# Kernel tuning notes

Hardware: AMD Instinct MI355X
Metric: run time of the kernel (lower is better)

Reference implementation:

```python
import jax, jax.numpy as jnp
import numpy as np

B, CH, T = 8, 512, 1024
HEADS = 8
KC = CH // HEADS  # 64
BLOCK = 256       # block_length


def setup_inputs() -> dict:
    key = jax.random.key(0)
    ks = jax.random.split(key, 10)
    s = 0.05
    x = jax.random.normal(ks[0], (B, CH, T), jnp.float32)
    c = jax.random.normal(ks[1], (B, CH, T), jnp.float32)
    attn_mask = jnp.ones((1, 1, T, T), jnp.int32)
    # 1x1 Conv1d weights are just [out, in] matrices over the channel dim.
    Wq = jax.random.normal(ks[2], (CH, CH), jnp.float32) * s
    bq = jax.random.normal(ks[3], (CH,), jnp.float32) * s
    Wk = jax.random.normal(ks[4], (CH, CH), jnp.float32) * s
    bk = jax.random.normal(ks[5], (CH,), jnp.float32) * s
    Wv = jax.random.normal(ks[6], (CH, CH), jnp.float32) * s
    bv = jax.random.normal(ks[7], (CH,), jnp.float32) * s
    Wo = jax.random.normal(ks[8], (CH, CH), jnp.float32) * s
    bo = jax.random.normal(ks[9], (CH,), jnp.float32) * s
    return {"x": x, "c": c, "attn_mask": attn_mask,
            "Wq": Wq, "bq": bq, "Wk": Wk, "bk": bk,
            "Wv": Wv, "bv": bv, "Wo": Wo, "bo": bo}


def _proj(W, b, z):
    # 1x1 Conv1d: [B,C,T] -> [B,O,T]
    return jnp.einsum('oc,bct->bot', W, z) + b[None, :, None]


def reference(x, c, attn_mask, Wq, bq, Wk, bk, Wv, bv, Wo, bo):
    q = _proj(Wq, bq, x)
    k = _proj(Wk, bk, c)
    v = _proj(Wv, bv, c)

    def split_heads(z):  # [B,C,T] -> [B,H,T,KC]
        return z.reshape(B, HEADS, KC, T).transpose(0, 1, 3, 2)

    qh, kh, vh = split_heads(q), split_heads(k), split_heads(v)

    scale = jnp.asarray(1.0 / np.sqrt(KC), qh.dtype)
    scores = jnp.einsum('bhtd,bhsd->bhts', qh * scale, kh)  # [B,H,T,T]

    r = jnp.arange(T)
    diff = jnp.abs(r[None, :] - r[:, None])  # |i - j|, [T,T]
    # proximal bias: -log(1 + |i-j|)
    scores = scores + (-jnp.log1p(diff.astype(scores.dtype)))[None, None]
    # attention mask: masked_fill(mask == 0, -1e4)
    scores = jnp.where(attn_mask == 0, jnp.asarray(-1e4, scores.dtype), scores)
    # block-length band mask: keep |i-j| <= BLOCK (triu(-BLOCK).tril(BLOCK))
    band = (diff <= BLOCK)[None, None]
    scores = jnp.where(band, scores, jnp.asarray(-1e4, scores.dtype))

    p_attn = jax.nn.softmax(scores, axis=-1)
    out = jnp.einsum('bhts,bhsd->bhtd', p_attn, vh)  # [B,H,T,KC]
    out = out.transpose(0, 1, 3, 2).reshape(B, CH, T)  # merge heads -> [B,C,T]
    return _proj(Wo, bo, out)
```

## Files before the change

kernel.cpp:

```cpp
#include <hip/hip_runtime.h>
#include <stdint.h>

typedef unsigned short u16;
typedef __attribute__((ext_vector_type(8))) __bf16 bf16x8;
typedef __attribute__((ext_vector_type(4))) float f32x4;

constexpr int B_ = 8, CH = 512, T = 1024, NH = 8, HD = 64, BAND = 256;

__device__ inline u16 f2b(float f) {
  union { float f; uint32_t u; } v; v.f = f;
  uint32_t r = (v.u + 0x7fffu + ((v.u >> 16) & 1u)) >> 16;
  return (u16)r;
}

__device__ inline f32x4 mfma16(bf16x8 a, bf16x8 b, f32x4 c) {
  return __builtin_amdgcn_mfma_f32_16x16x32_bf16(a, b, c, 0, 0, 0);
}

__device__ __forceinline__ void gld16(const void* g, void* l) {
  __builtin_amdgcn_global_load_lds((__attribute__((address_space(1))) void*)(g),
                                   (__attribute__((address_space(3))) void*)(l),
                                   16, 0, 0);
}

__device__ __forceinline__ float exp2_hw(float x) { return __builtin_amdgcn_exp2f(x); }

__global__ __launch_bounds__(256) void cvt_w(const float* __restrict__ wq, const float* __restrict__ wk,
                                             const float* __restrict__ wv, const float* __restrict__ wo,
                                             u16* __restrict__ out) {
  int idx = blockIdx.x * 256 + threadIdx.x;
  int w = idx >> 15;
  const float* src = (w == 0) ? wq : (w == 1) ? wk : (w == 2) ? wv : wo;
  int e = (idx & 32767) * 8;
  f32x4 a = *(const f32x4*)(src + e);
  f32x4 b = *(const f32x4*)(src + e + 4);
  union { u16 h[8]; bf16x8 v; } r;
  r.h[0] = f2b(a[0]); r.h[1] = f2b(a[1]); r.h[2] = f2b(a[2]); r.h[3] = f2b(a[3]);
  r.h[4] = f2b(b[0]); r.h[5] = f2b(b[1]); r.h[6] = f2b(b[2]); r.h[7] = f2b(b[3]);
  *(bf16x8*)(out + (w << 18) + e) = r.v;
}

__global__ __launch_bounds__(256) void tr_cvt(const float* __restrict__ x, const float* __restrict__ c,
                                              u16* __restrict__ xT, u16* __restrict__ cT) {
  __shared__ float tile[32][33];
  int z = blockIdx.z;
  const float* src = (z < B_) ? x : c;
  u16* dst = (z < B_) ? xT : cT;
  int b = (z < B_) ? z : z - B_;
  int t0 = blockIdx.x * 32, c0 = blockIdx.y * 32;
  int tx = threadIdx.x & 31, ty = threadIdx.x >> 5;
#pragma unroll
  for (int k = 0; k < 4; k++)
    tile[ty + 8 * k][tx] = src[(long)(b * CH + c0 + ty + 8 * k) * T + t0 + tx];
  __syncthreads();
#pragma unroll
  for (int k = 0; k < 4; k++)
    dst[(long)(b * T + t0 + ty + 8 * k) * CH + c0 + tx] = f2b(tile[tx][ty + 8 * k]);
}

template <int TN, typename OT>
__device__ __forceinline__ void gemm_core(const u16* __restrict__ Ab, int lda,
                                          const u16* __restrict__ Bb, int ldb,
                                          OT* __restrict__ Cb, int ldc,
                                          const float* __restrict__ bi, bool brow,
                                          int m0, int n0, int K, u16* smA, u16* smB) {
  int t = threadIdx.x, lane = t & 63, wave = t >> 6;
  int cl = lane & 15, quad = lane >> 4;
  int wm = wave >> 1, wn = wave & 1;
  int rr = t >> 3, gs = t & 7;
  constexpr int NW = TN / 32;
  f32x4 acc[4][NW] = {};
  for (int k0 = 0; k0 < K; k0 += 64) {
    __syncthreads();
#pragma unroll
    for (int j = 0; j < 4; j++) {
      int R = j * 32 + rr;
      int gc = (gs ^ (R & 7)) << 3;
      gld16(Ab + (long)(m0 + R) * lda + k0 + gc, (char*)smA + j * 4096 + wave * 1024);
      if (j < TN / 32)
        gld16(Bb + (long)(n0 + R) * ldb + k0 + gc, (char*)smB + j * 4096 + wave * 1024);
    }
    __syncthreads();
#pragma unroll
    for (int ks = 0; ks < 2; ks++) {
      int g2 = ((ks << 2) | quad) ^ (cl & 7);
      bf16x8 af[4], bb[NW];
#pragma unroll
      for (int i = 0; i < 4; i++)
        af[i] = *(const bf16x8*)&smA[(wm * 64 + i * 16 + cl) * 64 + g2 * 8];
#pragma unroll
      for (int i = 0; i < NW; i++)
        bb[i] = *(const bf16x8*)&smB[(wn * (TN / 2) + i * 16 + cl) * 64 + g2 * 8];
#pragma unroll
      for (int mi = 0; mi < 4; mi++)
#pragma unroll
        for (int ni = 0; ni < NW; ni++)
          acc[mi][ni] = mfma16(af[mi], bb[ni], acc[mi][ni]);
    }
  }
#pragma unroll
  for (int mi = 0; mi < 4; mi++) {
    int row = m0 + wm * 64 + mi * 16 + quad * 4;
#pragma unroll
    for (int ni = 0; ni < NW; ni++) {
      int col = n0 + wn * (TN / 2) + ni * 16 + cl;
#pragma unroll
      for (int r = 0; r < 4; r++) {
        float v = acc[mi][ni][r] + (brow ? bi[row + r] : bi[col]);
        if constexpr (sizeof(OT) == 2) Cb[(long)(row + r) * ldc + col] = f2b(v);
        else Cb[(long)(row + r) * ldc + col] = v;
      }
    }
  }
}

__global__ __launch_bounds__(256, 2) void gemm_qkv(const u16* __restrict__ xT, const u16* __restrict__ cT,
                                                   const u16* __restrict__ Wb,
                                                   u16* __restrict__ Qb, u16* __restrict__ Kb, u16* __restrict__ Vb,
                                                   const float* __restrict__ bq, const float* __restrict__ bk,
                                                   const float* __restrict__ bv) {
  __shared__ u16 smA[128 * 64], smB[128 * 64];
  const long TCH = (long)T * CH;
  int z = blockIdx.z, sec = z >> 3, zz = z & 7, bx = blockIdx.x;
  const u16 *Ab, *Bb; u16* Cb; const float* bi;
  int m0, n0, ldc; bool brow;
  if (sec == 0) {
    Ab = xT + zz * TCH; Bb = Wb;           Cb = Qb + zz * TCH;        bi = bq;
    m0 = (bx >> 2) * 128; n0 = (bx & 3) * 128; ldc = CH; brow = false;
  } else if (sec == 1) {
    Ab = cT + zz * TCH; Bb = Wb + 262144;  Cb = Kb + zz * TCH;        bi = bk;
    m0 = (bx >> 2) * 128; n0 = (bx & 3) * 128; ldc = CH; brow = false;
  } else {
    Ab = Wb + 2 * 262144; Bb = cT + zz * TCH; Cb = Vb + zz * (long)CH * T; bi = bv;
    m0 = (bx & 3) * 128; n0 = (bx >> 2) * 128; ldc = T; brow = true;
  }
  gemm_core<128, u16>(Ab, CH, Bb, CH, Cb, ldc, bi, brow, m0, n0, CH, smA, smB);
}

__global__ __launch_bounds__(256, 2) void gemm_o(const u16* __restrict__ Wo, const u16* __restrict__ AO,
                                                 float* __restrict__ out, const float* __restrict__ bo) {
  __shared__ u16 smA[128 * 64], smB[64 * 64];
  int z = blockIdx.z;
  gemm_core<64, float>(Wo, CH, AO + z * (long)T * CH, CH, out + z * (long)CH * T, T,
                       bo, true, blockIdx.y * 128, blockIdx.x * 64, CH, smA, smB);
}

__global__ __launch_bounds__(256, 4) void attn(const u16* __restrict__ Q, const u16* __restrict__ Kt,
                                               const u16* __restrict__ V, u16* __restrict__ AO) {
  __shared__ u16 pb[4][16][40];
  int lane = threadIdx.x & 63, wave = threadIdx.x >> 6;
  int cl = lane & 15, quad = lane >> 4;
  int bx = blockIdx.x;
  int xcd = bx & 7, ii = bx >> 3;
  int bh = xcd * 8 + (ii & 7);
  int qt = ii >> 3;
  int b = bh >> 3, h = bh & 7;
  int tq0 = qt * 64 + wave * 16;
  const u16* qb = Q + ((long)(b * T + tq0 + cl) * CH) + h * HD;
  bf16x8 qf0 = *(const bf16x8*)(qb + quad * 8);
  bf16x8 qf1 = *(const bf16x8*)(qb + 32 + quad * 8);
  f32x4 acc[4] = {};
  float lr[4] = {0.f, 0.f, 0.f, 0.f};
  float fir[4];
#pragma unroll
  for (int r = 0; r < 4; r++) fir[r] = (float)(tq0 + quad * 4 + r);
  int s_lo = tq0 - BAND; if (s_lo < 0) s_lo = 0; s_lo &= ~31;
  int s_hi = tq0 + 16 + BAND; if (s_hi > T) s_hi = T;

  const u16* kbase = Kt + ((long)(b * T + 2 * cl) * CH) + h * HD + quad * 8;
  const u16* vbase = V + ((long)(b * CH + h * HD + cl) * T) + quad * 8;
  bf16x8 kp[4], vp[4];
#define LOADK(j0, kk)                                                    \
  { const u16* kb = kbase + (long)(j0) * CH;                             \
    kk[0] = *(const bf16x8*)(kb);        kk[1] = *(const bf16x8*)(kb + 32); \
    kk[2] = *(const bf16x8*)(kb + CH);   kk[3] = *(const bf16x8*)(kb + CH + 32); }
#define LOADV(j0, vv)                                                    \
  { const u16* vb = vbase + (j0);                                        \
    vv[0] = *(const bf16x8*)(vb);              vv[1] = *(const bf16x8*)(vb + 16 * T); \
    vv[2] = *(const bf16x8*)(vb + 32 * T);     vv[3] = *(const bf16x8*)(vb + 48 * T); }
  LOADK(s_lo, kp); LOADV(s_lo, vp);

  float je = (float)(s_lo + 2 * cl);
  for (int j0 = s_lo; j0 < s_hi; j0 += 32, je += 32.f) {
    bf16x8 kc[4], vc[4];
#pragma unroll
    for (int i = 0; i < 4; i++) { kc[i] = kp[i]; vc[i] = vp[i]; }
    int jn = (j0 + 32 < s_hi) ? j0 + 32 : j0;
    LOADK(jn, kp); LOADV(jn, vp);
    f32x4 z = {0.f, 0.f, 0.f, 0.f};
    f32x4 s0 = mfma16(qf1, kc[1], mfma16(qf0, kc[0], z));
    f32x4 s1 = mfma16(qf1, kc[3], mfma16(qf0, kc[2], z));
#pragma unroll
    for (int r = 0; r < 4; r++) {
      float de = fabsf(fir[r] - je);
      float dd = fabsf(fir[r] - je - 1.f);
      constexpr float C2 = 0.125f * 1.4426950408889634f;
      float pe = exp2_hw(s0[r] * C2) * __builtin_amdgcn_rcpf(1.f + de);
      float po = exp2_hw(s1[r] * C2) * __builtin_amdgcn_rcpf(1.f + dd);
      pe = (de <= 256.f) ? pe : 0.f;
      po = (dd <= 256.f) ? po : 0.f;
      lr[r] += pe + po;
      uint32_t ue, uo;
      { union { float f; uint32_t u; } cv; cv.f = pe; ue = cv.u; cv.f = po; uo = cv.u; }
      uint32_t pk = ((uo + 0x8000u) & 0xffff0000u) | ((ue + 0x8000u) >> 16);
      *(uint32_t*)&pb[wave][quad * 4 + r][2 * cl] = pk;
    }
    bf16x8 pf = *(bf16x8*)&pb[wave][cl][quad * 8];
#pragma unroll
    for (int dg = 0; dg < 4; dg++)
      acc[dg] = mfma16(pf, vc[dg], acc[dg]);
  }
#undef LOADK
#undef LOADV
  float inv[4];
#pragma unroll
  for (int r = 0; r < 4; r++) {
    float s = lr[r];
    s += __shfl_xor(s, 1); s += __shfl_xor(s, 2);
    s += __shfl_xor(s, 4); s += __shfl_xor(s, 8);
    inv[r] = __builtin_amdgcn_rcpf(s);
  }
#pragma unroll
  for (int dg = 0; dg < 4; dg++)
#pragma unroll
    for (int r = 0; r < 4; r++)
      AO[((long)(b * T + tq0 + quad * 4 + r) * CH) + h * HD + dg * 16 + cl] = f2b(acc[dg][r] * inv[r]);
}

extern "C" void kernel_launch(void* const* d_in, const int* in_sizes, int n_in,
                              void* d_out, int out_size, void* d_ws, size_t ws_size,
                              hipStream_t stream) {
  const float* x  = (const float*)d_in[0];
  const float* c  = (const float*)d_in[1];
  const float* Wq = (const float*)d_in[3];
  const float* bq = (const float*)d_in[4];
  const float* Wk = (const float*)d_in[5];
  const float* bk = (const float*)d_in[6];
  const float* Wv = (const float*)d_in[7];
  const float* bv = (const float*)d_in[8];
  const float* Wo = (const float*)d_in[9];
  const float* bo = (const float*)d_in[10];
  float* out = (float*)d_out;

  const long NT = (long)B_ * T * CH;
  u16* Wb = (u16*)d_ws;
  u16* xT = Wb + 4 * 262144;
  u16* cT = xT + NT;
  u16* Qb = cT + NT;
  u16* Kb = Qb + NT;
  u16* Vb = Kb + NT;
  u16* AO = xT;

  cvt_w<<<dim3(512), dim3(256), 0, stream>>>(Wq, Wk, Wv, Wo, Wb);
  tr_cvt<<<dim3(32, 16, 16), dim3(256), 0, stream>>>(x, c, xT, cT);
  gemm_qkv<<<dim3(32, 1, 24), dim3(256), 0, stream>>>(xT, cT, Wb, Qb, Kb, Vb, bq, bk, bv);
  attn<<<dim3(1024), dim3(256), 0, stream>>>(Qb, Kb, Vb, AO);
  gemm_o<<<dim3(16, 4, 8), dim3(256), 0, stream>>>(Wb + 3 * 262144, AO, out, bo);
}
```

Baseline: 189.1 us.

## Stage K/V tiles in shared LDS with double-buffered async loads in attention

The attention kernel now loads 64-key K and V tiles once per block into XOR-swizzled LDS buffers using global_load_lds, double-buffered across iterations, and all four waves share them. Before, each wave streamed its own K/V fragments from global memory into registers. The intent is to remove the four-fold redundant global traffic per block and to overlap loads with compute. In exchange it adds a __syncthreads per tile and iterates over a union band that is wider than each wave's own band. It also changes the occupancy hints on all three kernels.

```diff
diff --git a/kernel.cpp b/kernel.cpp
--- a/kernel.cpp
+++ b/kernel.cpp
@@ -114,7 +114,7 @@
   }
 }
 
-__global__ __launch_bounds__(256, 2) void gemm_qkv(const u16* __restrict__ xT, const u16* __restrict__ cT,
+__global__ __launch_bounds__(256, 3) void gemm_qkv(const u16* __restrict__ xT, const u16* __restrict__ cT,
                                                    const u16* __restrict__ Wb,
                                                    u16* __restrict__ Qb, u16* __restrict__ Kb, u16* __restrict__ Vb,
                                                    const float* __restrict__ bq, const float* __restrict__ bk,
@@ -137,7 +137,7 @@
   gemm_core<128, u16>(Ab, CH, Bb, CH, Cb, ldc, bi, brow, m0, n0, CH, smA, smB);
 }
 
-__global__ __launch_bounds__(256, 2) void gemm_o(const u16* __restrict__ Wo, const u16* __restrict__ AO,
+__global__ __launch_bounds__(256, 4) void gemm_o(const u16* __restrict__ Wo, const u16* __restrict__ AO,
                                                  float* __restrict__ out, const float* __restrict__ bo) {
   __shared__ u16 smA[128 * 64], smB[64 * 64];
   int z = blockIdx.z;
@@ -145,9 +145,11 @@
                        bo, true, blockIdx.y * 128, blockIdx.x * 64, CH, smA, smB);
 }
 
-__global__ __launch_bounds__(256, 4) void attn(const u16* __restrict__ Q, const u16* __restrict__ Kt,
+__global__ __launch_bounds__(256, 3) void attn(const u16* __restrict__ Q, const u16* __restrict__ Kt,
                                                const u16* __restrict__ V, u16* __restrict__ AO) {
-  __shared__ u16 pb[4][16][40];
+  __shared__ u16 sK[2][64 * 64];
+  __shared__ u16 sV[2][64 * 64];
+  __shared__ u16 sP[4][16 * 72];
   int lane = threadIdx.x & 63, wave = threadIdx.x >> 6;
   int cl = lane & 15, quad = lane >> 4;
   int bx = blockIdx.x;
@@ -155,63 +157,85 @@
   int bh = xcd * 8 + (ii & 7);
   int qt = ii >> 3;
   int b = bh >> 3, h = bh & 7;
-  int tq0 = qt * 64 + wave * 16;
-  const u16* qb = Q + ((long)(b * T + tq0 + cl) * CH) + h * HD;
+  int tq0 = qt * 64;
+  int tqw = tq0 + wave * 16;
+  const u16* qb = Q + ((long)(b * T + tqw + cl) * CH) + h * HD;
   bf16x8 qf0 = *(const bf16x8*)(qb + quad * 8);
   bf16x8 qf1 = *(const bf16x8*)(qb + 32 + quad * 8);
   f32x4 acc[4] = {};
   float lr[4] = {0.f, 0.f, 0.f, 0.f};
   float fir[4];
 #pragma unroll
-  for (int r = 0; r < 4; r++) fir[r] = (float)(tq0 + quad * 4 + r);
-  int s_lo = tq0 - BAND; if (s_lo < 0) s_lo = 0; s_lo &= ~31;
-  int s_hi = tq0 + 16 + BAND; if (s_hi > T) s_hi = T;
-
-  const u16* kbase = Kt + ((long)(b * T + 2 * cl) * CH) + h * HD + quad * 8;
-  const u16* vbase = V + ((long)(b * CH + h * HD + cl) * T) + quad * 8;
-  bf16x8 kp[4], vp[4];
-#define LOADK(j0, kk)                                                    \
-  { const u16* kb = kbase + (long)(j0) * CH;                             \
-    kk[0] = *(const bf16x8*)(kb);        kk[1] = *(const bf16x8*)(kb + 32); \
-    kk[2] = *(const bf16x8*)(kb + CH);   kk[3] = *(const bf16x8*)(kb + CH + 32); }
-#define LOADV(j0, vv)                                                    \
-  { const u16* vb = vbase + (j0);                                        \
-    vv[0] = *(const bf16x8*)(vb);              vv[1] = *(const bf16x8*)(vb + 16 * T); \
-    vv[2] = *(const bf16x8*)(vb + 32 * T);     vv[3] = *(const bf16x8*)(vb + 48 * T); }
-  LOADK(s_lo, kp); LOADV(s_lo, vp);
-
-  float je = (float)(s_lo + 2 * cl);
-  for (int j0 = s_lo; j0 < s_hi; j0 += 32, je += 32.f) {
-    bf16x8 kc[4], vc[4];
-#pragma unroll
-    for (int i = 0; i < 4; i++) { kc[i] = kp[i]; vc[i] = vp[i]; }
-    int jn = (j0 + 32 < s_hi) ? j0 + 32 : j0;
-    LOADK(jn, kp); LOADV(jn, vp);
-    f32x4 z = {0.f, 0.f, 0.f, 0.f};
-    f32x4 s0 = mfma16(qf1, kc[1], mfma16(qf0, kc[0], z));
-    f32x4 s1 = mfma16(qf1, kc[3], mfma16(qf0, kc[2], z));
-#pragma unroll
-    for (int r = 0; r < 4; r++) {
-      float de = fabsf(fir[r] - je);
-      float dd = fabsf(fir[r] - je - 1.f);
-      constexpr float C2 = 0.125f * 1.4426950408889634f;
-      float pe = exp2_hw(s0[r] * C2) * __builtin_amdgcn_rcpf(1.f + de);
-      float po = exp2_hw(s1[r] * C2) * __builtin_amdgcn_rcpf(1.f + dd);
-      pe = (de <= 256.f) ? pe : 0.f;
-      po = (dd <= 256.f) ? po : 0.f;
-      lr[r] += pe + po;
-      uint32_t ue, uo;
-      { union { float f; uint32_t u; } cv; cv.f = pe; ue = cv.u; cv.f = po; uo = cv.u; }
-      uint32_t pk = ((uo + 0x8000u) & 0xffff0000u) | ((ue + 0x8000u) >> 16);
-      *(uint32_t*)&pb[wave][quad * 4 + r][2 * cl] = pk;
-    }
-    bf16x8 pf = *(bf16x8*)&pb[wave][cl][quad * 8];
-#pragma unroll
-    for (int dg = 0; dg < 4; dg++)
-      acc[dg] = mfma16(pf, vc[dg], acc[dg]);
-  }
-#undef LOADK
-#undef LOADV
+  for (int r = 0; r < 4; r++) fir[r] = (float)(tqw + quad * 4 + r);
+  int lo = tq0 - BAND; if (lo < 0) lo = 0;
+  int hi = tq0 + 64 + BAND; if (hi > T) hi = T;
+  int nt = (hi - lo) >> 6;
+
+  int rl = lane >> 3, cg = lane & 7;
+  const u16* ksrc = Kt + (long)b * T * CH + h * HD;
+  const u16* vsrc = V + ((long)(b * CH + h * HD) * T);
+
+#define STAGE(buf, j0)                                                          \
+  {                                                                             \
+    _Pragma("unroll")                                                           \
+    for (int i = 0; i < 2; i++) {                                               \
+      int r = wave * 16 + i * 8 + rl;                                           \
+      int s = ((r >> 5) << 5) + ((r >> 4) & 1) + ((r & 15) << 1);               \
+      gld16(ksrc + (long)(j0 + s) * CH + ((cg ^ (r & 7)) << 3),                 \
+            (char*)&sK[buf][(wave * 16 + i * 8) * 64]);                         \
+      gld16(vsrc + (long)r * T + (j0) + ((cg ^ (r & 7)) << 3),                  \
+            (char*)&sV[buf][(wave * 16 + i * 8) * 64]);                         \
+    }                                                                           \
+  }
+
+  STAGE(0, lo)
+  constexpr float C2 = 0.125f * 1.4426950408889634f;
+  for (int it = 0; it < nt; it++) {
+    int cur = it & 1;
+    int j0 = lo + it * 64;
+    __syncthreads();
+    if (it + 1 < nt) STAGE(1 - cur, j0 + 64)
+    f32x4 sg[2][2];
+#pragma unroll
+    for (int p = 0; p < 2; p++)
+#pragma unroll
+      for (int sub = 0; sub < 2; sub++) {
+        const u16* kr = &sK[cur][(p * 32 + sub * 16 + cl) * 64];
+        bf16x8 k0 = *(const bf16x8*)&kr[((quad ^ (cl & 7)) << 3)];
+        bf16x8 k1 = *(const bf16x8*)&kr[(((4 | quad) ^ (cl & 7)) << 3)];
+        f32x4 z = {0.f, 0.f, 0.f, 0.f};
+        sg[p][sub] = mfma16(qf1, k1, mfma16(qf0, k0, z));
+      }
+#pragma unroll
+    for (int p = 0; p < 2; p++) {
+      float jb = (float)(j0 + p * 32 + 2 * cl);
+#pragma unroll
+      for (int r = 0; r < 4; r++) {
+        float de = fabsf(fir[r] - jb);
+        float dd = fabsf(fir[r] - jb - 1.f);
+        float pe = exp2_hw(sg[p][0][r] * C2) * __builtin_amdgcn_rcpf(1.f + de);
+        float po = exp2_hw(sg[p][1][r] * C2) * __builtin_amdgcn_rcpf(1.f + dd);
+        pe = (de <= 256.f) ? pe : 0.f;
+        po = (dd <= 256.f) ? po : 0.f;
+        lr[r] += pe + po;
+        uint32_t ue, uo;
+        { union { float f; uint32_t u; } cv; cv.f = pe; ue = cv.u; cv.f = po; uo = cv.u; }
+        uint32_t pk = ((uo + 0x8000u) & 0xffff0000u) | ((ue + 0x8000u) >> 16);
+        *(uint32_t*)&sP[wave][(quad * 4 + r) * 72 + p * 32 + 2 * cl] = pk;
+      }
+    }
+#pragma unroll
+    for (int ks = 0; ks < 2; ks++) {
+      bf16x8 pf = *(bf16x8*)&sP[wave][cl * 72 + ks * 32 + quad * 8];
+#pragma unroll
+      for (int dg = 0; dg < 4; dg++) {
+        bf16x8 vf = *(const bf16x8*)&sV[cur][(dg * 16 + cl) * 64 +
+                                             ((((ks << 2) | quad) ^ (cl & 7)) << 3)];
+        acc[dg] = mfma16(pf, vf, acc[dg]);
+      }
+    }
+  }
+#undef STAGE
   float inv[4];
 #pragma unroll
   for (int r = 0; r < 4; r++) {
@@ -224,7 +248,7 @@
   for (int dg = 0; dg < 4; dg++)
 #pragma unroll
     for (int r = 0; r < 4; r++)
-      AO[((long)(b * T + tq0 + quad * 4 + r) * CH) + h * HD + dg * 16 + cl] = f2b(acc[dg][r] * inv[r]);
+      AO[((long)(b * T + tqw + quad * 4 + r) * CH) + h * HD + dg * 16 + cl] = f2b(acc[dg][r] * inv[r]);
 }
 
 extern "C" void kernel_launch(void* const* d_in, const int* in_sizes, int n_in,
```

After: 153.1 us. 1.23x faster.
